# Optimization experiments

Hardware: AMD Instinct MI355X
Metric: run time of the kernel (lower is better)

The kernel has to match this reference:

```python
import jax, jax.numpy as jnp
import numpy as np

B, C, H, W = 8, 2048, 14, 14
NUM_CLASSES, WORD_DIM, INTER_DIM = 80, 300, 1024


def setup_inputs() -> dict:
    key = jax.random.key(0)
    ks = jax.random.split(key, 8)
    s = 0.02
    return {
        "image_features": jax.random.normal(ks[0], (B, C, H, W), jnp.float32),
        "word_features": jax.random.normal(ks[1], (NUM_CLASSES, WORD_DIM), jnp.float32),
        "W1": jax.random.normal(ks[2], (INTER_DIM, C), jnp.float32) * s,
        "W2": jax.random.normal(ks[3], (INTER_DIM, WORD_DIM), jnp.float32) * s,
        "W3": jax.random.normal(ks[4], (INTER_DIM, INTER_DIM), jnp.float32) * s,
        "b3": jax.random.normal(ks[5], (INTER_DIM,), jnp.float32) * s,
        "Wa": jax.random.normal(ks[6], (1, INTER_DIM), jnp.float32) * s,
        "ba": jax.random.normal(ks[7], (1,), jnp.float32) * s,
        "num_classes": NUM_CLASSES,
    }


def reference(image_features, word_features, W1, W2, W3, b3, Wa, ba, num_classes):
    b, c, h, w = image_features.shape
    # [s, b, c] with s = h*w (spatial locations)
    img = image_features.reshape(b, c, h * w).transpose(2, 0, 1)
    f_wh = img @ W1.T                      # [s, b, D]
    f_wd = word_features @ W2.T            # [n, D]
    # additive-attention score MLP; broadcast to [s, b, n, D]
    lb = jnp.tanh(f_wh[:, :, None, :] * f_wd[None, None, :, :]) @ W3.T + b3
    coef = (lb @ Wa.T + ba)[..., 0]        # [s, b, n]
    coef = jax.nn.softmax(coef, axis=0)    # softmax over spatial locations
    # weighted sum over spatial dim -> [b, n, c]
    return jnp.einsum('sbc,sbn->bnc', img, coef)
```

## Files before the change

### kernel.cpp

```cpp
#include <hip/hip_runtime.h>
#include <math.h>

#define SB 196
#define SP 224
#define NB 8
#define NC 2048
#define ND 1024
#define NN 80
#define NW 300
#define CH 8
#define DCH (ND / CH)

typedef __bf16 v8bf __attribute__((ext_vector_type(8)));
typedef __bf16 v4bf __attribute__((ext_vector_type(4)));
typedef __bf16 v2bf __attribute__((ext_vector_type(2)));
typedef float  f32x4 __attribute__((ext_vector_type(4)));

__global__ __launch_bounds__(256) void k0_v(const float* __restrict__ W3,
                                            const float* __restrict__ Wa,
                                            float* __restrict__ v) {
    int d  = blockIdx.x * 256 + threadIdx.x;
    int e0 = blockIdx.y * 64;
    float p = 0.f;
    #pragma unroll 8
    for (int e = e0; e < e0 + 64; ++e) {
        p += Wa[e] * W3[(size_t)e * ND + d];
    }
    atomicAdd(&v[d], p);
}

__global__ __launch_bounds__(256) void k0_fwd(const float* __restrict__ word,
                                              const float* __restrict__ W2,
                                              const float* __restrict__ v,
                                              float2* __restrict__ wpack) {
    __shared__ __align__(16) float lword[NW];
    int n = blockIdx.x;
    int d = blockIdx.y * 256 + threadIdx.x;
    for (int i = threadIdx.x; i < NW; i += 256) lword[i] = word[(size_t)n * NW + i];
    __syncthreads();
    const float4* wr = (const float4*)(W2 + (size_t)d * NW);
    const float4* l4 = (const float4*)lword;
    float acc = 0.f;
    #pragma unroll 5
    for (int i = 0; i < NW / 4; ++i) {
        float4 a = wr[i], b = l4[i];
        acc += a.x * b.x + a.y * b.y + a.z * b.z + a.w * b.w;
    }
    float2 o;
    o.x = 2.8853900817779268f * acc;
    o.y = -2.f * v[d];
    wpack[(size_t)n * ND + d] = o;
}

__global__ __launch_bounds__(256) void kcast_x(const float* __restrict__ X,
                                               const float* __restrict__ W1,
                                               __bf16* __restrict__ Xt,
                                               __bf16* __restrict__ Xhi,
                                               __bf16* __restrict__ Xlo,
                                               __bf16* __restrict__ W1b) {
    const int t = threadIdx.x;
    if (blockIdx.z == 8) {
        unsigned int slice_tid = (blockIdx.x * 4 + blockIdx.y) * 256 + t;
        #pragma unroll 4
        for (int r = 0; r < 16; ++r) {
            size_t i = ((size_t)slice_tid + (size_t)r * 32768) * 4;
            float4 f = *(const float4*)(W1 + i);
            v4bf o;
            o[0] = (__bf16)f.x; o[1] = (__bf16)f.y;
            o[2] = (__bf16)f.z; o[3] = (__bf16)f.w;
            *(v4bf*)(W1b + i) = o;
        }
        return;
    }
    __shared__ float tile[64][65];
    const int b  = blockIdx.z;
    const int c0 = blockIdx.x * 64;
    const int s0 = blockIdx.y * 64;
    const float* Xb = X + (size_t)b * NC * SB;
    {
        int ss = t & 63, cbase = t >> 6;
        #pragma unroll
        for (int r = 0; r < 16; ++r) {
            int cc = cbase + 4 * r;
            float val = (s0 + ss < SB) ? Xb[(size_t)(c0 + cc) * SB + s0 + ss] : 0.f;
            tile[cc][ss] = val;
        }
    }
    __syncthreads();
    {
        int cc = t & 63, sbase = t >> 6;
        #pragma unroll
        for (int r = 0; r < 16; ++r) {
            int ss = sbase + 4 * r;
            if (s0 + ss < SB)
                Xt[((size_t)b * SB + s0 + ss) * NC + c0 + cc] = (__bf16)tile[cc][ss];
        }
    }
    {
        int ss = t & 63, cbase = t >> 6;
        int sg = s0 + ss;
        #pragma unroll
        for (int r = 0; r < 16; ++r) {
            int cc = cbase + 4 * r;
            if (sg < SP) {
                float val = (sg < SB) ? tile[cc][ss] : 0.f;
                __bf16 h = (__bf16)val;
                __bf16 l = (__bf16)(val - (float)h);
                size_t base = ((size_t)b * NC + c0 + cc) * SP + sg;
                Xhi[base] = h;
                Xlo[base] = l;
            }
        }
    }
}

#define PITCH 40
__global__ __launch_bounds__(256) void k1_mfma(const __bf16* __restrict__ Xt,
                                               const __bf16* __restrict__ W1b,
                                               float* __restrict__ F) {
    __shared__ __align__(16) __bf16 lA[64 * PITCH];
    __shared__ __align__(16) __bf16 lB[64 * PITCH];
    const int t    = threadIdx.x;
    const int d0   = blockIdx.x * 64;
    const int s0   = blockIdx.y * 64;
    const int b    = blockIdx.z;
    const int lane = t & 63;
    const int wave = t >> 6;
    const int doff = (wave & 1) * 32;
    const int soff = (wave >> 1) * 32;
    const int quad = lane >> 4;
    const int l16  = lane & 15;

    f32x4 acc[2][2] = {};

    const int rr = t >> 2;
    const int cc = (t & 3) * 8;
    const bool sv = (s0 + rr) < SB;
    const __bf16* Ag = W1b + (size_t)(d0 + rr) * NC + cc;
    const __bf16* Bg = Xt + ((size_t)b * SB + (sv ? (s0 + rr) : 0)) * NC + cc;
    __bf16* lAw = lA + rr * PITCH + cc;
    __bf16* lBw = lB + rr * PITCH + cc;

    const __bf16* rA0 = lA + (doff + l16) * PITCH + quad * 8;
    const __bf16* rA1 = rA0 + 16 * PITCH;
    const __bf16* rB0 = lB + (soff + l16) * PITCH + quad * 8;
    const __bf16* rB1 = rB0 + 16 * PITCH;

    for (int k0 = 0; k0 < NC; k0 += 32) {
        uint4 a = *(const uint4*)(Ag + k0);
        uint4 bv = sv ? *(const uint4*)(Bg + k0) : make_uint4(0u, 0u, 0u, 0u);
        __syncthreads();
        *(uint4*)lAw = a;
        *(uint4*)lBw = bv;
        __syncthreads();
        v8bf a0 = *(const v8bf*)rA0;
        v8bf a1 = *(const v8bf*)rA1;
        v8bf b0 = *(const v8bf*)rB0;
        v8bf b1 = *(const v8bf*)rB1;
        acc[0][0] = __builtin_amdgcn_mfma_f32_16x16x32_bf16(a0, b0, acc[0][0], 0, 0, 0);
        acc[0][1] = __builtin_amdgcn_mfma_f32_16x16x32_bf16(a0, b1, acc[0][1], 0, 0, 0);
        acc[1][0] = __builtin_amdgcn_mfma_f32_16x16x32_bf16(a1, b0, acc[1][0], 0, 0, 0);
        acc[1][1] = __builtin_amdgcn_mfma_f32_16x16x32_bf16(a1, b1, acc[1][1], 0, 0, 0);
    }
    float* Fb = F + (size_t)b * ND * SB;
    #pragma unroll
    for (int i = 0; i < 2; ++i) {
        #pragma unroll
        for (int j = 0; j < 2; ++j) {
            int s = s0 + soff + j * 16 + l16;
            if (s < SB) {
                #pragma unroll
                for (int r = 0; r < 4; ++r) {
                    int d = d0 + doff + i * 16 + quad * 4 + r;
                    Fb[(size_t)d * SB + s] = acc[i][j][r];
                }
            }
        }
    }
}

__global__ __launch_bounds__(256) void k2a(const float* __restrict__ F,
                                           const float2* __restrict__ wpack,
                                           float* __restrict__ part) {
    const int n0  = blockIdx.x * 4;
    const int ch  = blockIdx.z;
    const int idx = blockIdx.y * 256 + threadIdx.x;
    const bool valid = idx < (NB * SB);
    const int iv = valid ? idx : 0;
    const int b  = iv / SB;
    const int s  = iv - b * SB;
    const float*  Fp  = F + ((size_t)b * ND + ch * DCH) * SB + s;
    const float4* wp0 = (const float4*)(wpack + (size_t)(n0 + 0) * ND + ch * DCH);
    const float4* wp1 = (const float4*)(wpack + (size_t)(n0 + 1) * ND + ch * DCH);
    const float4* wp2 = (const float4*)(wpack + (size_t)(n0 + 2) * ND + ch * DCH);
    const float4* wp3 = (const float4*)(wpack + (size_t)(n0 + 3) * ND + ch * DCH);
    float a0 = 0.f, a1 = 0.f, a2 = 0.f, a3 = 0.f;
    #pragma unroll 4
    for (int d2 = 0; d2 < DCH / 2; ++d2) {
        float f0 = Fp[(size_t)(2 * d2)     * SB];
        float f1 = Fp[(size_t)(2 * d2 + 1) * SB];
        float4 w0 = wp0[d2];
        float4 w1 = wp1[d2];
        float4 w2 = wp2[d2];
        float4 w3 = wp3[d2];
        float e00 = __builtin_amdgcn_exp2f(f0 * w0.x);
        float e01 = __builtin_amdgcn_exp2f(f1 * w0.z);
        float e10 = __builtin_amdgcn_exp2f(f0 * w1.x);
        float e11 = __builtin_amdgcn_exp2f(f1 * w1.z);
        float e20 = __builtin_amdgcn_exp2f(f0 * w2.x);
        float e21 = __builtin_amdgcn_exp2f(f1 * w2.z);
        float e30 = __builtin_amdgcn_exp2f(f0 * w3.x);
        float e31 = __builtin_amdgcn_exp2f(f1 * w3.z);
        a0 = fmaf(w0.y, __builtin_amdgcn_rcpf(1.f + e00), a0);
        a0 = fmaf(w0.w, __builtin_amdgcn_rcpf(1.f + e01), a0);
        a1 = fmaf(w1.y, __builtin_amdgcn_rcpf(1.f + e10), a1);
        a1 = fmaf(w1.w, __builtin_amdgcn_rcpf(1.f + e11), a1);
        a2 = fmaf(w2.y, __builtin_amdgcn_rcpf(1.f + e20), a2);
        a2 = fmaf(w2.w, __builtin_amdgcn_rcpf(1.f + e21), a2);
        a3 = fmaf(w3.y, __builtin_amdgcn_rcpf(1.f + e30), a3);
        a3 = fmaf(w3.w, __builtin_amdgcn_rcpf(1.f + e31), a3);
    }
    if (valid) {
        size_t base = ((size_t)ch * NB + b) * NN;
        part[(base + n0 + 0) * 256 + s] = a0;
        part[(base + n0 + 1) * 256 + s] = a1;
        part[(base + n0 + 2) * 256 + s] = a2;
        part[(base + n0 + 3) * 256 + s] = a3;
    }
}

__global__ __launch_bounds__(256) void k2b(const float* __restrict__ part,
                                           __bf16* __restrict__ coefh,
                                           __bf16* __restrict__ coefl) {
    __shared__ float red[256];
    const int n = blockIdx.x;
    const int b = blockIdx.y;
    const int t = threadIdx.x;
    float acc = 0.f;
    #pragma unroll
    for (int ch = 0; ch < CH; ++ch)
        acc += part[(((size_t)ch * NB + b) * NN + n) * 256 + t];

    red[t] = (t < SB) ? acc : -1e30f;
    __syncthreads();
    #pragma unroll
    for (int off = 128; off > 0; off >>= 1) {
        if (t < off) red[t] = fmaxf(red[t], red[t + off]);
        __syncthreads();
    }
    float m = red[0];
    __syncthreads();
    float p = (t < SB) ? __expf(acc - m) : 0.f;
    red[t] = p;
    __syncthreads();
    #pragma unroll
    for (int off = 128; off > 0; off >>= 1) {
        if (t < off) red[t] += red[t + off];
        __syncthreads();
    }
    float inv = 1.f / red[0];
    if (t < SP) {
        float val = (t < SB) ? p * inv : 0.f;
        __bf16 h = (__bf16)val;
        __bf16 l = (__bf16)(val - (float)h);
        size_t base = ((size_t)b * NN + n) * SP + t;
        coefh[base] = h;
        coefl[base] = l;
    }
}

__global__ __launch_bounds__(256) void k3_mfma(const __bf16* __restrict__ Xhi,
                                               const __bf16* __restrict__ Xlo,
                                               const __bf16* __restrict__ coefh,
                                               const __bf16* __restrict__ coefl,
                                               float* __restrict__ out) {
    const int t     = threadIdx.x;
    const int wave  = t >> 6;
    const int lane  = t & 63;
    const int quad  = lane >> 4;
    const int l16   = lane & 15;
    const int b     = blockIdx.y;
    const int cbase = blockIdx.x * 64 + wave * 16;

    const __bf16* Bh = Xhi + ((size_t)b * NC + cbase + l16) * SP + quad * 8;
    const __bf16* Bl = Xlo + ((size_t)b * NC + cbase + l16) * SP + quad * 8;
    const __bf16* Ah = coefh + ((size_t)b * NN + l16) * SP + quad * 8;
    const __bf16* Al = coefl + ((size_t)b * NN + l16) * SP + quad * 8;

    f32x4 acc[5] = {};

    #pragma unroll
    for (int k0 = 0; k0 < SP; k0 += 32) {
        v8bf bh = *(const v8bf*)(Bh + k0);
        v8bf bl = *(const v8bf*)(Bl + k0);
        #pragma unroll
        for (int mt = 0; mt < 5; ++mt) {
            v8bf ah = *(const v8bf*)(Ah + (size_t)mt * 16 * SP + k0);
            v8bf al = *(const v8bf*)(Al + (size_t)mt * 16 * SP + k0);
            acc[mt] = __builtin_amdgcn_mfma_f32_16x16x32_bf16(ah, bh, acc[mt], 0, 0, 0);
            acc[mt] = __builtin_amdgcn_mfma_f32_16x16x32_bf16(al, bh, acc[mt], 0, 0, 0);
            acc[mt] = __builtin_amdgcn_mfma_f32_16x16x32_bf16(ah, bl, acc[mt], 0, 0, 0);
        }
    }
    #pragma unroll
    for (int mt = 0; mt < 5; ++mt) {
        #pragma unroll
        for (int r = 0; r < 4; ++r) {
            int n = mt * 16 + quad * 4 + r;
            out[((size_t)b * NN + n) * NC + cbase + l16] = acc[mt][r];
        }
    }
}

extern "C" void kernel_launch(void* const* d_in, const int* in_sizes, int n_in,
                              void* d_out, int out_size, void* d_ws, size_t ws_size,
                              hipStream_t stream) {
    const float* X    = (const float*)d_in[0];
    const float* word = (const float*)d_in[1];
    const float* W1   = (const float*)d_in[2];
    const float* W2   = (const float*)d_in[3];
    const float* W3   = (const float*)d_in[4];
    const float* Wa   = (const float*)d_in[6];
    float* out = (float*)d_out;

    char* ws = (char*)d_ws;
    float*  v     = (float*)ws;
    float2* wpack = (float2*)(v + ND);
    float*  part  = (float*)(wpack + (size_t)NN * ND);
    __bf16* coefh = (__bf16*)(part + (size_t)CH * NB * NN * 256);
    __bf16* coefl = coefh + (size_t)NB * NN * SP;
    __bf16* W1b   = coefl + (size_t)NB * NN * SP;
    __bf16* Xt    = W1b + (size_t)ND * NC;
    float*  F     = (float*)(Xt + (size_t)NB * SB * NC);
    __bf16* Xhi   = (__bf16*)(F + (size_t)NB * ND * SB);
    __bf16* Xlo   = Xhi + (size_t)NB * NC * SP;

    hipMemsetAsync(v, 0, ND * sizeof(float), stream);
    k0_v   <<<dim3(4, 16),       256, 0, stream>>>(W3, Wa, v);
    k0_fwd <<<dim3(NN, 4),       256, 0, stream>>>(word, W2, v, wpack);
    kcast_x<<<dim3(32, 4, 9),    256, 0, stream>>>(X, W1, Xt, Xhi, Xlo, W1b);
    k1_mfma<<<dim3(16, 4, NB),   256, 0, stream>>>(Xt, W1b, F);
    k2a    <<<dim3(NN / 4, 7, CH), 256, 0, stream>>>(F, wpack, part);
    k2b    <<<dim3(NN, NB),      256, 0, stream>>>(part, coefh, coefl);
    k3_mfma<<<dim3(NC / 64, NB), 256, 0, stream>>>(Xhi, Xlo, coefh, coefl, out);
}
```

Baseline: 190.0 us.

## Fold small precompute kernels into cast and GEMM launches, flatten batch in GEMM

Drops the memset and the two small setup kernels. The v reduction now runs as extra blocks of the cast kernel and writes partial sums instead of using atomics. The word projection runs as an extra row of blocks in the first GEMM, which sums those partials. The GEMM now treats batch and spatial as one flattened dimension over zero-padded rows, so fewer tiles are wasted on padding, and it loads tiles with global_load_lds direct-to-LDS copies. This cuts launch count and register staging, but puts slow scalar work inside the GEMM grid and drops the LDS pitch padding, which may cause bank conflicts.

Measured after the change: 288.3 us. 1.52x slower.

```diff
diff --git a/kernel.cpp b/kernel.cpp
--- a/kernel.cpp
+++ b/kernel.cpp
@@ -10,55 +10,47 @@
 #define NW 300
 #define CH 8
 #define DCH (ND / CH)
+#define NJ (NB * SB)
+#define NJP 1600
 
 typedef __bf16 v8bf __attribute__((ext_vector_type(8)));
 typedef __bf16 v4bf __attribute__((ext_vector_type(4)));
-typedef __bf16 v2bf __attribute__((ext_vector_type(2)));
 typedef float  f32x4 __attribute__((ext_vector_type(4)));
 
-__global__ __launch_bounds__(256) void k0_v(const float* __restrict__ W3,
-                                            const float* __restrict__ Wa,
-                                            float* __restrict__ v) {
-    int d  = blockIdx.x * 256 + threadIdx.x;
-    int e0 = blockIdx.y * 64;
-    float p = 0.f;
-    #pragma unroll 8
-    for (int e = e0; e < e0 + 64; ++e) {
-        p += Wa[e] * W3[(size_t)e * ND + d];
-    }
-    atomicAdd(&v[d], p);
-}
-
-__global__ __launch_bounds__(256) void k0_fwd(const float* __restrict__ word,
-                                              const float* __restrict__ W2,
-                                              const float* __restrict__ v,
-                                              float2* __restrict__ wpack) {
-    __shared__ __align__(16) float lword[NW];
-    int n = blockIdx.x;
-    int d = blockIdx.y * 256 + threadIdx.x;
-    for (int i = threadIdx.x; i < NW; i += 256) lword[i] = word[(size_t)n * NW + i];
-    __syncthreads();
-    const float4* wr = (const float4*)(W2 + (size_t)d * NW);
-    const float4* l4 = (const float4*)lword;
-    float acc = 0.f;
-    #pragma unroll 5
-    for (int i = 0; i < NW / 4; ++i) {
-        float4 a = wr[i], b = l4[i];
-        acc += a.x * b.x + a.y * b.y + a.z * b.z + a.w * b.w;
-    }
-    float2 o;
-    o.x = 2.8853900817779268f * acc;
-    o.y = -2.f * v[d];
-    wpack[(size_t)n * ND + d] = o;
+__device__ __forceinline__ void gload16(const __bf16* g, __bf16* l) {
+    __builtin_amdgcn_global_load_lds(
+        (const __attribute__((address_space(1))) void*)g,
+        (__attribute__((address_space(3))) void*)l, 16, 0, 0);
 }
 
 __global__ __launch_bounds__(256) void kcast_x(const float* __restrict__ X,
                                                const float* __restrict__ W1,
+                                               const float* __restrict__ W3,
+                                               const float* __restrict__ Wa,
                                                __bf16* __restrict__ Xt,
                                                __bf16* __restrict__ Xhi,
                                                __bf16* __restrict__ Xlo,
-                                               __bf16* __restrict__ W1b) {
+                                               __bf16* __restrict__ W1b,
+                                               float* __restrict__ vpart) {
     const int t = threadIdx.x;
+    if (blockIdx.z == 9) {
+        if (blockIdx.x < 16) {
+            const int e0 = blockIdx.x * 64;
+            const int d  = blockIdx.y * 256 + t;
+            float p = 0.f;
+            #pragma unroll 8
+            for (int e = e0; e < e0 + 64; ++e)
+                p += Wa[e] * W3[(size_t)e * ND + d];
+            vpart[blockIdx.x * ND + d] = p;
+        } else if (blockIdx.x == 16) {
+            const int tid = blockIdx.y * 256 + t;
+            uint4 z = make_uint4(0u, 0u, 0u, 0u);
+            uint4* p = (uint4*)(Xt + (size_t)NJ * NC);
+            #pragma unroll
+            for (int r = 0; r < 8; ++r) p[tid + r * 1024] = z;
+        }
+        return;
+    }
     if (blockIdx.z == 8) {
         unsigned int slice_tid = (blockIdx.x * 4 + blockIdx.y) * 256 + t;
         #pragma unroll 4
@@ -114,44 +106,68 @@
     }
 }
 
-#define PITCH 40
 __global__ __launch_bounds__(256) void k1_mfma(const __bf16* __restrict__ Xt,
                                                const __bf16* __restrict__ W1b,
-                                               float* __restrict__ F) {
-    __shared__ __align__(16) __bf16 lA[64 * PITCH];
-    __shared__ __align__(16) __bf16 lB[64 * PITCH];
+                                               float* __restrict__ F,
+                                               const float* __restrict__ word,
+                                               const float* __restrict__ W2,
+                                               const float* __restrict__ vpart,
+                                               float2* __restrict__ wpack) {
+    if (blockIdx.y == 25) {
+        const int g = blockIdx.x * 256 + threadIdx.x;
+        #pragma unroll 1
+        for (int u = 0; u < 20; ++u) {
+            int flat = u * 4096 + g;
+            int n = flat >> 10;
+            int d = flat & 1023;
+            const float4* wr = (const float4*)(W2 + (size_t)d * NW);
+            const float4* wd = (const float4*)(word + (size_t)n * NW);
+            float acc = 0.f;
+            #pragma unroll 5
+            for (int i = 0; i < NW / 4; ++i) {
+                float4 a = wr[i], b = wd[i];
+                acc += a.x * b.x + a.y * b.y + a.z * b.z + a.w * b.w;
+            }
+            float vv = 0.f;
+            #pragma unroll
+            for (int p = 0; p < 16; ++p) vv += vpart[p * ND + d];
+            float2 o;
+            o.x = 2.8853900817779268f * acc;
+            o.y = -2.f * vv;
+            wpack[(size_t)n * ND + d] = o;
+        }
+        return;
+    }
+    __shared__ __align__(16) __bf16 lA[64 * 32];
+    __shared__ __align__(16) __bf16 lB[64 * 32];
     const int t    = threadIdx.x;
     const int d0   = blockIdx.x * 64;
-    const int s0   = blockIdx.y * 64;
-    const int b    = blockIdx.z;
+    const int j0   = blockIdx.y * 64;
     const int lane = t & 63;
     const int wave = t >> 6;
     const int doff = (wave & 1) * 32;
-    const int soff = (wave >> 1) * 32;
+    const int joff = (wave >> 1) * 32;
     const int quad = lane >> 4;
     const int l16  = lane & 15;
 
     f32x4 acc[2][2] = {};
 
-    const int rr = t >> 2;
-    const int cc = (t & 3) * 8;
-    const bool sv = (s0 + rr) < SB;
-    const __bf16* Ag = W1b + (size_t)(d0 + rr) * NC + cc;
-    const __bf16* Bg = Xt + ((size_t)b * SB + (sv ? (s0 + rr) : 0)) * NC + cc;
-    __bf16* lAw = lA + rr * PITCH + cc;
-    __bf16* lBw = lB + rr * PITCH + cc;
-
-    const __bf16* rA0 = lA + (doff + l16) * PITCH + quad * 8;
-    const __bf16* rA1 = rA0 + 16 * PITCH;
-    const __bf16* rB0 = lB + (soff + l16) * PITCH + quad * 8;
-    const __bf16* rB1 = rB0 + 16 * PITCH;
+    const int srow   = wave * 16 + (lane >> 2);
+    const int schunk = (lane & 3) * 8;
+    const __bf16* Ag = W1b + (size_t)(d0 + srow) * NC + schunk;
+    const __bf16* Bg = Xt + (size_t)(j0 + srow) * NC + schunk;
+    __bf16* lAw = lA + wave * 512;
+    __bf16* lBw = lB + wave * 512;
+
+    const __bf16* rA0 = lA + (doff + l16) * 32 + quad * 8;
+    const __bf16* rA1 = rA0 + 16 * 32;
+    const __bf16* rB0 = lB + (joff + l16) * 32 + quad * 8;
+    const __bf16* rB1 = rB0 + 16 * 32;
 
     for (int k0 = 0; k0 < NC; k0 += 32) {
-        uint4 a = *(const uint4*)(Ag + k0);
-        uint4 bv = sv ? *(const uint4*)(Bg + k0) : make_uint4(0u, 0u, 0u, 0u);
         __syncthreads();
-        *(uint4*)lAw = a;
-        *(uint4*)lBw = bv;
+        gload16(Ag + k0, lAw);
+        gload16(Bg + k0, lBw);
         __syncthreads();
         v8bf a0 = *(const v8bf*)rA0;
         v8bf a1 = *(const v8bf*)rA1;
@@ -162,18 +178,18 @@
         acc[1][0] = __builtin_amdgcn_mfma_f32_16x16x32_bf16(a1, b0, acc[1][0], 0, 0, 0);
         acc[1][1] = __builtin_amdgcn_mfma_f32_16x16x32_bf16(a1, b1, acc[1][1], 0, 0, 0);
     }
-    float* Fb = F + (size_t)b * ND * SB;
     #pragma unroll
     for (int i = 0; i < 2; ++i) {
         #pragma unroll
-        for (int j = 0; j < 2; ++j) {
-            int s = s0 + soff + j * 16 + l16;
-            if (s < SB) {
+        for (int jj = 0; jj < 2; ++jj) {
+            int j = j0 + joff + jj * 16 + l16;
+            if (j < NJ) {
+                int b = j / SB;
+                int s = j - b * SB;
+                float* Fp = F + ((size_t)b * ND + d0 + doff + i * 16 + quad * 4) * SB + s;
                 #pragma unroll
-                for (int r = 0; r < 4; ++r) {
-                    int d = d0 + doff + i * 16 + quad * 4 + r;
-                    Fb[(size_t)d * SB + s] = acc[i][j][r];
-                }
+                for (int r = 0; r < 4; ++r)
+                    Fp[(size_t)r * SB] = acc[i][jj][r];
             }
         }
     }
@@ -324,22 +340,19 @@
     float* out = (float*)d_out;
 
     char* ws = (char*)d_ws;
-    float*  v     = (float*)ws;
-    float2* wpack = (float2*)(v + ND);
+    float*  vpart = (float*)ws;
+    float2* wpack = (float2*)(vpart + 16 * ND);
     float*  part  = (float*)(wpack + (size_t)NN * ND);
     __bf16* coefh = (__bf16*)(part + (size_t)CH * NB * NN * 256);
     __bf16* coefl = coefh + (size_t)NB * NN * SP;
     __bf16* W1b   = coefl + (size_t)NB * NN * SP;
     __bf16* Xt    = W1b + (size_t)ND * NC;
-    float*  F     = (float*)(Xt + (size_t)NB * SB * NC);
+    float*  F     = (float*)(Xt + (size_t)NJP * NC);
     __bf16* Xhi   = (__bf16*)(F + (size_t)NB * ND * SB);
     __bf16* Xlo   = Xhi + (size_t)NB * NC * SP;
 
-    hipMemsetAsync(v, 0, ND * sizeof(float), stream);
-    k0_v   <<<dim3(4, 16),       256, 0, stream>>>(W3, Wa, v);
-    k0_fwd <<<dim3(NN, 4),       256, 0, stream>>>(word, W2, v, wpack);
-    kcast_x<<<dim3(32, 4, 9),    256, 0, stream>>>(X, W1, Xt, Xhi, Xlo, W1b);
-    k1_mfma<<<dim3(16, 4, NB),   256, 0, stream>>>(Xt, W1b, F);
+    kcast_x<<<dim3(32, 4, 10),   256, 0, stream>>>(X, W1, W3, Wa, Xt, Xhi, Xlo, W1b, vpart);
+    k1_mfma<<<dim3(16, 26),      256, 0, stream>>>(Xt, W1b, F, word, W2, vpart, wpack);
     k2a    <<<dim3(NN / 4, 7, CH), 256, 0, stream>>>(F, wpack, part);
     k2b    <<<dim3(NN, NB),      256, 0, stream>>>(part, coefh, coefl);
     k3_mfma<<<dim3(NC / 64, NB), 256, 0, stream>>>(Xhi, Xlo, coefh, coefl, out);
```
